# Performance work log

Measured on AMD Instinct MI355X. Metric: run time of the kernel, lower is better.

Reference implementation:

```python
import jax, jax.numpy as jnp
import numpy as np

H = 128      # num_hidden
HIN = 384    # num_in (h_E feature dim)
DFF = 512    # FFN inner dim = 4*H
SCALE = 30.0
EPS = 1e-5

def gelu(x):
    return jax.nn.gelu(x, approximate=False)

def linear(x, w, b):
    return x @ w.T + b

def layer_norm(x, w, b):
    mu = jnp.mean(x, axis=-1, keepdims=True)
    var = jnp.var(x, axis=-1, keepdims=True)
    return (x - mu) * jax.lax.rsqrt(var + EPS) * w + b


def setup_inputs() -> dict:
    key = jax.random.key(0)
    ks = jax.random.split(key, 10)
    B, N, K = 4, 2048, 48
    s = lambda d: 1.0 / np.sqrt(d)
    return {
        "h_V": jax.random.normal(ks[0], (B, N, H), jnp.float32),
        "h_E": jax.random.normal(ks[1], (B, N, K, HIN), jnp.float32),
        "mask_V": jnp.ones((B, N), jnp.float32),
        "mask_attend": jnp.ones((B, N, K), jnp.float32),
        "W1_w": jax.random.normal(ks[2], (H, H + HIN), jnp.float32) * s(H + HIN),
        "W1_b": jnp.zeros((H,), jnp.float32),
        "W2_w": jax.random.normal(ks[3], (H, H), jnp.float32) * s(H),
        "W2_b": jnp.zeros((H,), jnp.float32),
        "W3_w": jax.random.normal(ks[4], (H, H), jnp.float32) * s(H),
        "W3_b": jnp.zeros((H,), jnp.float32),
        "ln1_w": jnp.ones((H,), jnp.float32),
        "ln1_b": jnp.zeros((H,), jnp.float32),
        "Win_w": jax.random.normal(ks[5], (DFF, H), jnp.float32) * s(H),
        "Win_b": jnp.zeros((DFF,), jnp.float32),
        "Wout_w": jax.random.normal(ks[6], (H, DFF), jnp.float32) * s(DFF),
        "Wout_b": jnp.zeros((H,), jnp.float32),
        "ln2_w": jnp.ones((H,), jnp.float32),
        "ln2_b": jnp.zeros((H,), jnp.float32),
    }


def reference(h_V, h_E, mask_V, mask_attend,
              W1_w, W1_b, W2_w, W2_b, W3_w, W3_b,
              ln1_w, ln1_b, Win_w, Win_b, Wout_w, Wout_b, ln2_w, ln2_b):
    K = h_E.shape[-2]
    # broadcast node feats to neighbors and concat: [B, N, K, H+HIN]
    h_V_expand = jnp.broadcast_to(h_V[:, :, None, :], (*h_V.shape[:2], K, h_V.shape[-1]))
    h_EV = jnp.concatenate([h_V_expand, h_E], axis=-1)
    h_message = linear(gelu(linear(gelu(linear(h_EV, W1_w, W1_b)), W2_w, W2_b)), W3_w, W3_b)
    h_message = mask_attend[..., None] * h_message
    dh = jnp.sum(h_message, axis=-2) / SCALE
    h = layer_norm(h_V + dh, ln1_w, ln1_b)
    dh = linear(gelu(linear(h, Win_w, Win_b)), Wout_w, Wout_b)
    h = layer_norm(h + dh, ln2_w, ln2_b)
    return mask_V[..., None] * h
```

## Files before the change

kernel.cpp:

```cpp
#include <hip/hip_runtime.h>
#include <hip/hip_bf16.h>

#define H    128
#define HIN  384
#define FIN  512
#define KNB  48
#define DFF  512
#define NNODES 8192
#define NNB_F (KNB*HIN)

typedef float f32x4 __attribute__((ext_vector_type(4)));
typedef short bf16x8 __attribute__((ext_vector_type(8)));

__device__ __forceinline__ short bfs(float x){
  __hip_bfloat16 h = __float2bfloat16(x);
  return *(short*)&h;
}

__device__ __forceinline__ bf16x8 pack8(float4 a, float4 b){
  bf16x8 o;
  o[0]=bfs(a.x); o[1]=bfs(a.y); o[2]=bfs(a.z); o[3]=bfs(a.w);
  o[4]=bfs(b.x); o[5]=bfs(b.y); o[6]=bfs(b.z); o[7]=bfs(b.w);
  return o;
}

__device__ __forceinline__ float gelu_f(float x){
  float x2 = x*x;
  float z  = x * fmaf(0.0713548162726f, x2, 1.59576912161f);
  z = fminf(fmaxf(z, -30.f), 30.f);
  float e = __expf(z);
  return x * e * __builtin_amdgcn_rcpf(1.f + e);
}

__device__ __forceinline__ f32x4 zero4(){ f32x4 z; z[0]=0.f;z[1]=0.f;z[2]=0.f;z[3]=0.f; return z; }

__global__ __launch_bounds__(256) void k_convert(
    const float* __restrict__ W1, const float* __restrict__ W2,
    const float* __restrict__ W3, const float* __restrict__ Win,
    const float* __restrict__ Wout, unsigned short* __restrict__ dst)
{
  int i0 = (blockIdx.x*256 + threadIdx.x)*4;
  #pragma unroll
  for (int t=0;t<4;t++){
    int idx = i0 + t;
    float v;
    if      (idx <  65536) v = W1[idx];
    else if (idx <  81920) v = W2[idx-65536];
    else if (idx <  98304) v = W3[idx-81920];
    else if (idx < 163840) v = Win[idx-98304];
    else                   v = Wout[idx-163840];
    dst[idx] = (unsigned short)bfs(v);
  }
}

__global__ __launch_bounds__(256) void k_bias1(
    const float* __restrict__ hV, const unsigned short* __restrict__ wW1,
    const float* __restrict__ W1b, float* __restrict__ bias1)
{
  int tid = threadIdx.x;
  int wid = tid>>6, lane = tid&63;
  int lr = lane&15, lg = lane>>4;
  int m0 = (blockIdx.x*4 + wid)*16;

  f32x4 acc[8];
  #pragma unroll
  for (int i=0;i<8;i++) acc[i] = zero4();

  #pragma unroll
  for (int ks=0; ks<4; ks++){
    const float* p = hV + (size_t)(m0+lr)*H + ks*32 + lg*8;
    bf16x8 a = pack8(*(const float4*)p, *(const float4*)(p+4));
    #pragma unroll
    for (int nt=0; nt<8; nt++){
      bf16x8 b = *(const bf16x8*)(wW1 + (size_t)(nt*16+lr)*FIN + ks*32 + lg*8);
      acc[nt] = __builtin_amdgcn_mfma_f32_16x16x32_bf16(a, b, acc[nt], 0,0,0);
    }
  }
  #pragma unroll
  for (int nt=0; nt<8; nt++){
    int col = nt*16 + lr;
    float bv = W1b[col];
    #pragma unroll
    for (int e=0;e<4;e++){
      int row = lg*4 + e;
      bias1[(size_t)(m0+row)*H + col] = acc[nt][e] + bv;
    }
  }
}

__global__ __launch_bounds__(256,5) void k_message(
    const float* __restrict__ hV, const float* __restrict__ hE,
    const float* __restrict__ maskA,
    const unsigned short* __restrict__ wW1, const unsigned short* __restrict__ wW2,
    const unsigned short* __restrict__ wW3,
    const float* __restrict__ W2b, const float* __restrict__ W3b,
    const float* __restrict__ ln1w, const float* __restrict__ ln1b,
    const float* __restrict__ bias1, float* __restrict__ hmid)
{
  __shared__ __align__(16) unsigned short sB0[48*136];
  __shared__ __align__(16) unsigned short sB1[48*136];
  __shared__ float sMask[48];
  __shared__ float sBias[128];
  __shared__ float sDh[128];

  int node = blockIdx.x;
  int tid  = threadIdx.x;
  const float* hEn = hE + (size_t)node * NNB_F;

  int wid = tid>>6, lane = tid&63;
  int lr = lane&15, lg = lane>>4;
  int sr = tid>>4, scg = tid&15;
  const float* gp = hEn + sr*HIN + scg*8;

  float4 pf[3][2];
  #pragma unroll
  for (int i=0;i<3;i++){
    const float* p = gp + i*16*HIN;
    pf[i][0] = *(const float4*)(p); pf[i][1] = *(const float4*)(p+4);
  }
  if (tid < 48)  sMask[tid] = maskA[(size_t)node*KNB + tid];
  if (tid < 128) sBias[tid] = bias1[(size_t)node*H + tid];
  #pragma unroll
  for (int i=0;i<3;i++)
    *(bf16x8*)(&sB0[(sr+16*i)*136 + scg*8]) = pack8(pf[i][0], pf[i][1]);
  __syncthreads();

  f32x4 acc1[3][2];
  #pragma unroll
  for (int mt=0;mt<3;mt++){ acc1[mt][0]=zero4(); acc1[mt][1]=zero4(); }

  auto gemm1_chunk = [&](const unsigned short* buf, int c){
    #pragma unroll
    for (int ks=0; ks<4; ks++){
      bf16x8 a[3];
      #pragma unroll
      for (int mt=0;mt<3;mt++)
        a[mt] = *(const bf16x8*)(buf + (mt*16+lr)*136 + ks*32 + lg*8);
      #pragma unroll
      for (int j=0;j<2;j++){
        int nt = wid*2 + j;
        bf16x8 b = *(const bf16x8*)(wW1 + (size_t)(nt*16+lr)*FIN + (H + c*128 + ks*32 + lg*8));
        #pragma unroll
        for (int mt=0;mt<3;mt++)
          acc1[mt][j] = __builtin_amdgcn_mfma_f32_16x16x32_bf16(a[mt], b, acc1[mt][j], 0,0,0);
      }
    }
  };

  #pragma unroll
  for (int i=0;i<3;i++){
    const float* p = gp + i*16*HIN + 128;
    pf[i][0] = *(const float4*)(p); pf[i][1] = *(const float4*)(p+4);
  }
  gemm1_chunk(sB0, 0);
  #pragma unroll
  for (int i=0;i<3;i++)
    *(bf16x8*)(&sB1[(sr+16*i)*136 + scg*8]) = pack8(pf[i][0], pf[i][1]);
  __syncthreads();

  #pragma unroll
  for (int i=0;i<3;i++){
    const float* p = gp + i*16*HIN + 256;
    pf[i][0] = *(const float4*)(p); pf[i][1] = *(const float4*)(p+4);
  }
  gemm1_chunk(sB1, 1);
  #pragma unroll
  for (int i=0;i<3;i++)
    *(bf16x8*)(&sB0[(sr+16*i)*136 + scg*8]) = pack8(pf[i][0], pf[i][1]);
  __syncthreads();

  gemm1_chunk(sB0, 2);

  #pragma unroll
  for (int j=0;j<2;j++){
    int col = (wid*2+j)*16 + lr;
    float bv = sBias[col];
    #pragma unroll
    for (int mt=0;mt<3;mt++){
      #pragma unroll
      for (int e=0;e<4;e++){
        float g = gelu_f(acc1[mt][j][e] + bv);
        int row = mt*16 + lg*4 + e;
        sB1[row*136 + col] = (unsigned short)bfs(g);
      }
    }
  }
  __syncthreads();

  f32x4 acc2[3][2];
  #pragma unroll
  for (int mt=0;mt<3;mt++){ acc2[mt][0]=zero4(); acc2[mt][1]=zero4(); }
  #pragma unroll
  for (int ks=0; ks<4; ks++){
    bf16x8 a[3];
    #pragma unroll
    for (int mt=0;mt<3;mt++)
      a[mt] = *(const bf16x8*)(sB1 + (mt*16+lr)*136 + ks*32 + lg*8);
    #pragma unroll
    for (int j=0;j<2;j++){
      int nt = wid*2 + j;
      bf16x8 b = *(const bf16x8*)(wW2 + (size_t)(nt*16+lr)*H + ks*32 + lg*8);
      #pragma unroll
      for (int mt=0;mt<3;mt++)
        acc2[mt][j] = __builtin_amdgcn_mfma_f32_16x16x32_bf16(a[mt], b, acc2[mt][j], 0,0,0);
    }
  }
  #pragma unroll
  for (int j=0;j<2;j++){
    int col = (wid*2+j)*16 + lr;
    float bv = W2b[col];
    #pragma unroll
    for (int mt=0;mt<3;mt++){
      #pragma unroll
      for (int e=0;e<4;e++){
        float g = gelu_f(acc2[mt][j][e] + bv);
        int row = mt*16 + lg*4 + e;
        sB0[row*136 + col] = (unsigned short)bfs(g);
      }
    }
  }
  __syncthreads();

  f32x4 acc3[3][2];
  #pragma unroll
  for (int mt=0;mt<3;mt++){ acc3[mt][0]=zero4(); acc3[mt][1]=zero4(); }
  #pragma unroll
  for (int ks=0; ks<4; ks++){
    bf16x8 a[3];
    #pragma unroll
    for (int mt=0;mt<3;mt++)
      a[mt] = *(const bf16x8*)(sB0 + (mt*16+lr)*136 + ks*32 + lg*8);
    #pragma unroll
    for (int j=0;j<2;j++){
      int nt = wid*2 + j;
      bf16x8 b = *(const bf16x8*)(wW3 + (size_t)(nt*16+lr)*H + ks*32 + lg*8);
      #pragma unroll
      for (int mt=0;mt<3;mt++)
        acc3[mt][j] = __builtin_amdgcn_mfma_f32_16x16x32_bf16(a[mt], b, acc3[mt][j], 0,0,0);
    }
  }
  #pragma unroll
  for (int j=0;j<2;j++){
    int col = (wid*2+j)*16 + lr;
    float bv = W3b[col];
    float p = 0.f;
    #pragma unroll
    for (int mt=0;mt<3;mt++){
      #pragma unroll
      for (int e=0;e<4;e++){
        int row = mt*16 + lg*4 + e;
        p += (acc3[mt][j][e] + bv) * sMask[row];
      }
    }
    p += __shfl_xor(p, 16);
    p += __shfl_xor(p, 32);
    if (lane < 16) sDh[(wid*2+j)*16 + lane] = p;
  }
  __syncthreads();

  if (wid == 0){
    int c0i = lane, c1i = lane + 64;
    float t0 = hV[(size_t)node*H + c0i] + sDh[c0i]*(1.0f/30.0f);
    float t1 = hV[(size_t)node*H + c1i] + sDh[c1i]*(1.0f/30.0f);
    float s = t0 + t1, q = t0*t0 + t1*t1;
    #pragma unroll
    for (int off=1; off<64; off<<=1){ s += __shfl_xor(s, off); q += __shfl_xor(q, off); }
    float mu  = s * (1.0f/128.0f);
    float var = q * (1.0f/128.0f) - mu*mu;
    float rs  = rsqrtf(var + 1e-5f);
    hmid[(size_t)node*H + c0i] = (t0-mu)*rs*ln1w[c0i] + ln1b[c0i];
    hmid[(size_t)node*H + c1i] = (t1-mu)*rs*ln1w[c1i] + ln1b[c1i];
  }
}

__global__ __launch_bounds__(256) void k_ffn(
    const float* __restrict__ hmid, const unsigned short* __restrict__ wWin,
    const unsigned short* __restrict__ wWout,
    const float* __restrict__ Winb, const float* __restrict__ Woutb,
    const float* __restrict__ ln2w, const float* __restrict__ ln2b,
    const float* __restrict__ maskV, float* __restrict__ out)
{
  __shared__ __align__(16) unsigned short sH[32*136];
  __shared__ __align__(16) unsigned short sU[32*520];
  __shared__ float sT[32*132];

  int tid = threadIdx.x;
  int m0 = blockIdx.x * 32;

  #pragma unroll
  for (int i=0;i<2;i++){
    int c = i*256 + tid;
    int row = c>>4, cir = c&15;
    const float* p = hmid + (size_t)(m0+row)*H + cir*8;
    *(bf16x8*)(sH + row*136 + cir*8) = pack8(*(const float4*)p, *(const float4*)(p+4));
  }
  __syncthreads();

  int wid = tid>>6, lane = tid&63;
  int lr = lane&15, lg = lane>>4;

  f32x4 acc[2][8];
  #pragma unroll
  for (int mt=0;mt<2;mt++)
    #pragma unroll
    for (int j=0;j<8;j++) acc[mt][j] = zero4();

  #pragma unroll
  for (int ks=0; ks<4; ks++){
    bf16x8 a[2];
    #pragma unroll
    for (int mt=0;mt<2;mt++)
      a[mt] = *(const bf16x8*)(sH + (mt*16+lr)*136 + ks*32 + lg*8);
    #pragma unroll
    for (int j=0;j<8;j++){
      int nt = wid*8 + j;
      bf16x8 b = *(const bf16x8*)(wWin + (size_t)(nt*16+lr)*H + ks*32 + lg*8);
      #pragma unroll
      for (int mt=0;mt<2;mt++)
        acc[mt][j] = __builtin_amdgcn_mfma_f32_16x16x32_bf16(a[mt], b, acc[mt][j], 0,0,0);
    }
  }
  #pragma unroll
  for (int j=0;j<8;j++){
    int col = (wid*8+j)*16 + lr;
    float bv = Winb[col];
    #pragma unroll
    for (int mt=0;mt<2;mt++){
      #pragma unroll
      for (int e=0;e<4;e++){
        float g = gelu_f(acc[mt][j][e] + bv);
        int row = mt*16 + lg*4 + e;
        sU[row*520 + col] = (unsigned short)bfs(g);
      }
    }
  }
  __syncthreads();

  f32x4 accO[2][2];
  #pragma unroll
  for (int mt=0;mt<2;mt++){ accO[mt][0]=zero4(); accO[mt][1]=zero4(); }

  for (int ks=0; ks<16; ks++){
    bf16x8 a[2];
    #pragma unroll
    for (int mt=0;mt<2;mt++)
      a[mt] = *(const bf16x8*)(sU + (mt*16+lr)*520 + ks*32 + lg*8);
    #pragma unroll
    for (int j=0;j<2;j++){
      int nt = wid*2 + j;
      bf16x8 b = *(const bf16x8*)(wWout + (size_t)(nt*16+lr)*DFF + ks*32 + lg*8);
      #pragma unroll
      for (int mt=0;mt<2;mt++)
        accO[mt][j] = __builtin_amdgcn_mfma_f32_16x16x32_bf16(a[mt], b, accO[mt][j], 0,0,0);
    }
  }
  #pragma unroll
  for (int j=0;j<2;j++){
    int col = (wid*2+j)*16 + lr;
    float bv = Woutb[col];
    #pragma unroll
    for (int mt=0;mt<2;mt++){
      #pragma unroll
      for (int e=0;e<4;e++){
        int row = mt*16 + lg*4 + e;
        float t = accO[mt][j][e] + bv + hmid[(size_t)(m0+row)*H + col];
        sT[row*132 + col] = t;
      }
    }
  }
  __syncthreads();

  int row = tid>>3, part = tid&7;
  float s=0.f, q=0.f;
  #pragma unroll
  for (int jj=0;jj<16;jj++){
    float v = sT[row*132 + part*16 + jj];
    s += v; q += v*v;
  }
  s += __shfl_xor(s,1); q += __shfl_xor(q,1);
  s += __shfl_xor(s,2); q += __shfl_xor(q,2);
  s += __shfl_xor(s,4); q += __shfl_xor(q,4);
  float mu  = s*(1.0f/128.0f);
  float var = q*(1.0f/128.0f) - mu*mu;
  float rs  = rsqrtf(var + 1e-5f);
  float mv  = maskV[m0+row];
  #pragma unroll
  for (int jj=0;jj<16;jj++){
    int c = part*16 + jj;
    out[(size_t)(m0+row)*H + c] = mv * ((sT[row*132+c]-mu)*rs*ln2w[c] + ln2b[c]);
  }
}

extern "C" void kernel_launch(void* const* d_in, const int* in_sizes, int n_in,
                              void* d_out, int out_size, void* d_ws, size_t ws_size,
                              hipStream_t stream)
{
  const float* hV    = (const float*)d_in[0];
  const float* hE    = (const float*)d_in[1];
  const float* maskV = (const float*)d_in[2];
  const float* maskA = (const float*)d_in[3];
  const float* W1w   = (const float*)d_in[4];
  const float* W1b   = (const float*)d_in[5];
  const float* W2w   = (const float*)d_in[6];
  const float* W2b   = (const float*)d_in[7];
  const float* W3w   = (const float*)d_in[8];
  const float* W3b   = (const float*)d_in[9];
  const float* ln1w  = (const float*)d_in[10];
  const float* ln1b  = (const float*)d_in[11];
  const float* Winw  = (const float*)d_in[12];
  const float* Winb  = (const float*)d_in[13];
  const float* Woutw = (const float*)d_in[14];
  const float* Woutb = (const float*)d_in[15];
  const float* ln2w  = (const float*)d_in[16];
  const float* ln2b  = (const float*)d_in[17];

  unsigned short* wAll  = (unsigned short*)d_ws;
  unsigned short* wW1   = wAll;
  unsigned short* wW2   = wAll + 65536;
  unsigned short* wW3   = wAll + 81920;
  unsigned short* wWin  = wAll + 98304;
  unsigned short* wWout = wAll + 163840;
  float* bias1 = (float*)((char*)d_ws + 458752);
  float* hmid  = (float*)d_out;
  float* outp  = (float*)d_out;

  k_convert<<<224, 256, 0, stream>>>(W1w, W2w, W3w, Winw, Woutw, wAll);
  k_bias1  <<<128, 256, 0, stream>>>(hV, wW1, W1b, bias1);
  k_message<<<NNODES, 256, 0, stream>>>(hV, hE, maskA, wW1, wW2, wW3,
                                        W2b, W3b, ln1w, ln1b, bias1, hmid);
  k_ffn    <<<NNODES/32, 256, 0, stream>>>(hmid, wWin, wWout, Winb, Woutb,
                                           ln2w, ln2b, maskV, outp);
}
```

Before: 249.7 us.

## Assign one node per wavefront in message kernel, replacing block barriers with wave fences

Each wavefront now processes a whole node on its own: all 128 output columns per GEMM, with a private LDS tile. This replaces the block-wide __syncthreads and the shared double buffer with wave-local LDS fences, and the grid shrinks by four. The goal is to remove block-level synchronisation stalls and let each wave stream its own h_E. The cost is 96 accumulator registers per wave (launch bounds lowered to 3), and the global loads are no longer prefetched ahead of the MFMA work.

```diff
diff --git a/kernel.cpp b/kernel.cpp
--- a/kernel.cpp
+++ b/kernel.cpp
@@ -33,6 +33,11 @@
 }
 
 __device__ __forceinline__ f32x4 zero4(){ f32x4 z; z[0]=0.f;z[1]=0.f;z[2]=0.f;z[3]=0.f; return z; }
+
+__device__ __forceinline__ void wave_lds_fence(){
+  asm volatile("s_waitcnt lgkmcnt(0)" ::: "memory");
+  __builtin_amdgcn_wave_barrier();
+}
 
 __global__ __launch_bounds__(256) void k_convert(
     const float* __restrict__ W1, const float* __restrict__ W2,
@@ -88,7 +93,7 @@
   }
 }
 
-__global__ __launch_bounds__(256,5) void k_message(
+__global__ __launch_bounds__(256,3) void k_message(
     const float* __restrict__ hV, const float* __restrict__ hE,
     const float* __restrict__ maskA,
     const unsigned short* __restrict__ wW1, const unsigned short* __restrict__ wW2,
@@ -97,168 +102,148 @@
     const float* __restrict__ ln1w, const float* __restrict__ ln1b,
     const float* __restrict__ bias1, float* __restrict__ hmid)
 {
-  __shared__ __align__(16) unsigned short sB0[48*136];
-  __shared__ __align__(16) unsigned short sB1[48*136];
-  __shared__ float sMask[48];
-  __shared__ float sBias[128];
-  __shared__ float sDh[128];
-
-  int node = blockIdx.x;
+  __shared__ __align__(16) unsigned short sWave[4][48*136];
+
   int tid  = threadIdx.x;
+  int wid  = tid>>6, lane = tid&63;
+  int node = blockIdx.x*4 + wid;
+  unsigned short* sG = sWave[wid];
+
+  int lr = lane&15, lg = lane>>4;
+  int srow = lane>>4, scol = lane&15;
   const float* hEn = hE + (size_t)node * NNB_F;
 
-  int wid = tid>>6, lane = tid&63;
-  int lr = lane&15, lg = lane>>4;
-  int sr = tid>>4, scg = tid&15;
-  const float* gp = hEn + sr*HIN + scg*8;
-
-  float4 pf[3][2];
-  #pragma unroll
-  for (int i=0;i<3;i++){
-    const float* p = gp + i*16*HIN;
-    pf[i][0] = *(const float4*)(p); pf[i][1] = *(const float4*)(p+4);
-  }
-  if (tid < 48)  sMask[tid] = maskA[(size_t)node*KNB + tid];
-  if (tid < 128) sBias[tid] = bias1[(size_t)node*H + tid];
-  #pragma unroll
-  for (int i=0;i<3;i++)
-    *(bf16x8*)(&sB0[(sr+16*i)*136 + scg*8]) = pack8(pf[i][0], pf[i][1]);
-  __syncthreads();
-
-  f32x4 acc1[3][2];
-  #pragma unroll
-  for (int mt=0;mt<3;mt++){ acc1[mt][0]=zero4(); acc1[mt][1]=zero4(); }
-
-  auto gemm1_chunk = [&](const unsigned short* buf, int c){
+  f32x4 acc[3][8];
+  #pragma unroll
+  for (int mt=0;mt<3;mt++)
+    #pragma unroll
+    for (int nt=0;nt<8;nt++) acc[mt][nt] = zero4();
+
+  for (int c=0;c<3;++c){
+    const float* cp = hEn + c*128 + scol*8;
+    #pragma unroll
+    for (int i=0;i<12;i++){
+      int row = srow + 4*i;
+      const float* p = cp + (size_t)row*HIN;
+      float4 a0 = *(const float4*)p, a1 = *(const float4*)(p+4);
+      *(bf16x8*)(sG + row*136 + scol*8) = pack8(a0, a1);
+    }
+    wave_lds_fence();
+
     #pragma unroll
     for (int ks=0; ks<4; ks++){
       bf16x8 a[3];
       #pragma unroll
       for (int mt=0;mt<3;mt++)
-        a[mt] = *(const bf16x8*)(buf + (mt*16+lr)*136 + ks*32 + lg*8);
-      #pragma unroll
-      for (int j=0;j<2;j++){
-        int nt = wid*2 + j;
+        a[mt] = *(const bf16x8*)(sG + (mt*16+lr)*136 + ks*32 + lg*8);
+      #pragma unroll
+      for (int nt=0;nt<8;nt++){
         bf16x8 b = *(const bf16x8*)(wW1 + (size_t)(nt*16+lr)*FIN + (H + c*128 + ks*32 + lg*8));
         #pragma unroll
         for (int mt=0;mt<3;mt++)
-          acc1[mt][j] = __builtin_amdgcn_mfma_f32_16x16x32_bf16(a[mt], b, acc1[mt][j], 0,0,0);
+          acc[mt][nt] = __builtin_amdgcn_mfma_f32_16x16x32_bf16(a[mt], b, acc[mt][nt], 0,0,0);
       }
     }
-  };
-
-  #pragma unroll
-  for (int i=0;i<3;i++){
-    const float* p = gp + i*16*HIN + 128;
-    pf[i][0] = *(const float4*)(p); pf[i][1] = *(const float4*)(p+4);
-  }
-  gemm1_chunk(sB0, 0);
-  #pragma unroll
-  for (int i=0;i<3;i++)
-    *(bf16x8*)(&sB1[(sr+16*i)*136 + scg*8]) = pack8(pf[i][0], pf[i][1]);
-  __syncthreads();
-
-  #pragma unroll
-  for (int i=0;i<3;i++){
-    const float* p = gp + i*16*HIN + 256;
-    pf[i][0] = *(const float4*)(p); pf[i][1] = *(const float4*)(p+4);
-  }
-  gemm1_chunk(sB1, 1);
-  #pragma unroll
-  for (int i=0;i<3;i++)
-    *(bf16x8*)(&sB0[(sr+16*i)*136 + scg*8]) = pack8(pf[i][0], pf[i][1]);
-  __syncthreads();
-
-  gemm1_chunk(sB0, 2);
-
-  #pragma unroll
-  for (int j=0;j<2;j++){
-    int col = (wid*2+j)*16 + lr;
-    float bv = sBias[col];
-    #pragma unroll
-    for (int mt=0;mt<3;mt++){
+    wave_lds_fence();
+  }
+
+  #pragma unroll
+  for (int nt=0;nt<8;nt++){
+    float bv = bias1[(size_t)node*H + nt*16 + lr];
+    #pragma unroll
+    for (int mt=0;mt<3;mt++)
       #pragma unroll
       for (int e=0;e<4;e++){
-        float g = gelu_f(acc1[mt][j][e] + bv);
-        int row = mt*16 + lg*4 + e;
-        sB1[row*136 + col] = (unsigned short)bfs(g);
+        float g = gelu_f(acc[mt][nt][e] + bv);
+        sG[(mt*16+lg*4+e)*136 + nt*16+lr] = (unsigned short)bfs(g);
       }
-    }
-  }
-  __syncthreads();
-
-  f32x4 acc2[3][2];
-  #pragma unroll
-  for (int mt=0;mt<3;mt++){ acc2[mt][0]=zero4(); acc2[mt][1]=zero4(); }
+  }
+  wave_lds_fence();
+
+  f32x4 acc2[3][8];
+  #pragma unroll
+  for (int mt=0;mt<3;mt++)
+    #pragma unroll
+    for (int nt=0;nt<8;nt++) acc2[mt][nt] = zero4();
   #pragma unroll
   for (int ks=0; ks<4; ks++){
     bf16x8 a[3];
     #pragma unroll
     for (int mt=0;mt<3;mt++)
-      a[mt] = *(const bf16x8*)(sB1 + (mt*16+lr)*136 + ks*32 + lg*8);
-    #pragma unroll
-    for (int j=0;j<2;j++){
-      int nt = wid*2 + j;
+      a[mt] = *(const bf16x8*)(sG + (mt*16+lr)*136 + ks*32 + lg*8);
+    #pragma unroll
+    for (int nt=0;nt<8;nt++){
       bf16x8 b = *(const bf16x8*)(wW2 + (size_t)(nt*16+lr)*H + ks*32 + lg*8);
       #pragma unroll
       for (int mt=0;mt<3;mt++)
-        acc2[mt][j] = __builtin_amdgcn_mfma_f32_16x16x32_bf16(a[mt], b, acc2[mt][j], 0,0,0);
-    }
-  }
-  #pragma unroll
-  for (int j=0;j<2;j++){
-    int col = (wid*2+j)*16 + lr;
-    float bv = W2b[col];
-    #pragma unroll
-    for (int mt=0;mt<3;mt++){
+        acc2[mt][nt] = __builtin_amdgcn_mfma_f32_16x16x32_bf16(a[mt], b, acc2[mt][nt], 0,0,0);
+    }
+  }
+  wave_lds_fence();
+
+  #pragma unroll
+  for (int nt=0;nt<8;nt++){
+    float bv = W2b[nt*16 + lr];
+    #pragma unroll
+    for (int mt=0;mt<3;mt++)
       #pragma unroll
       for (int e=0;e<4;e++){
-        float g = gelu_f(acc2[mt][j][e] + bv);
-        int row = mt*16 + lg*4 + e;
-        sB0[row*136 + col] = (unsigned short)bfs(g);
+        float g = gelu_f(acc2[mt][nt][e] + bv);
+        sG[(mt*16+lg*4+e)*136 + nt*16+lr] = (unsigned short)bfs(g);
       }
-    }
-  }
-  __syncthreads();
-
-  f32x4 acc3[3][2];
-  #pragma unroll
-  for (int mt=0;mt<3;mt++){ acc3[mt][0]=zero4(); acc3[mt][1]=zero4(); }
+  }
+  wave_lds_fence();
+
+  f32x4 acc3[3][8];
+  #pragma unroll
+  for (int mt=0;mt<3;mt++)
+    #pragma unroll
+    for (int nt=0;nt<8;nt++) acc3[mt][nt] = zero4();
   #pragma unroll
   for (int ks=0; ks<4; ks++){
     bf16x8 a[3];
     #pragma unroll
     for (int mt=0;mt<3;mt++)
-      a[mt] = *(const bf16x8*)(sB0 + (mt*16+lr)*136 + ks*32 + lg*8);
-    #pragma unroll
-    for (int j=0;j<2;j++){
-      int nt = wid*2 + j;
+      a[mt] = *(const bf16x8*)(sG + (mt*16+lr)*136 + ks*32 + lg*8);
+    #pragma unroll
+    for (int nt=0;nt<8;nt++){
       bf16x8 b = *(const bf16x8*)(wW3 + (size_t)(nt*16+lr)*H + ks*32 + lg*8);
       #pragma unroll
       for (int mt=0;mt<3;mt++)
-        acc3[mt][j] = __builtin_amdgcn_mfma_f32_16x16x32_bf16(a[mt], b, acc3[mt][j], 0,0,0);
-    }
-  }
-  #pragma unroll
-  for (int j=0;j<2;j++){
-    int col = (wid*2+j)*16 + lr;
-    float bv = W3b[col];
+        acc3[mt][nt] = __builtin_amdgcn_mfma_f32_16x16x32_bf16(a[mt], b, acc3[mt][nt], 0,0,0);
+    }
+  }
+  wave_lds_fence();
+
+  float mv[3][4];
+  #pragma unroll
+  for (int mt=0;mt<3;mt++)
+    #pragma unroll
+    for (int e=0;e<4;e++)
+      mv[mt][e] = maskA[(size_t)node*KNB + mt*16 + lg*4 + e];
+
+  float pn[8];
+  #pragma unroll
+  for (int nt=0;nt<8;nt++){
+    float bv = W3b[nt*16 + lr];
     float p = 0.f;
     #pragma unroll
-    for (int mt=0;mt<3;mt++){
-      #pragma unroll
-      for (int e=0;e<4;e++){
-        int row = mt*16 + lg*4 + e;
-        p += (acc3[mt][j][e] + bv) * sMask[row];
-      }
-    }
+    for (int mt=0;mt<3;mt++)
+      #pragma unroll
+      for (int e=0;e<4;e++)
+        p += (acc3[mt][nt][e] + bv) * mv[mt][e];
     p += __shfl_xor(p, 16);
     p += __shfl_xor(p, 32);
-    if (lane < 16) sDh[(wid*2+j)*16 + lane] = p;
-  }
-  __syncthreads();
-
-  if (wid == 0){
+    pn[nt] = p;
+  }
+  float* sDh = (float*)sG;
+  if (lane < 16){
+    #pragma unroll
+    for (int nt=0;nt<8;nt++) sDh[nt*16 + lane] = pn[nt];
+  }
+  wave_lds_fence();
+
+  {
     int c0i = lane, c1i = lane + 64;
     float t0 = hV[(size_t)node*H + c0i] + sDh[c0i]*(1.0f/30.0f);
     float t1 = hV[(size_t)node*H + c1i] + sDh[c1i]*(1.0f/30.0f);
@@ -426,8 +411,8 @@
 
   k_convert<<<224, 256, 0, stream>>>(W1w, W2w, W3w, Winw, Woutw, wAll);
   k_bias1  <<<128, 256, 0, stream>>>(hV, wW1, W1b, bias1);
-  k_message<<<NNODES, 256, 0, stream>>>(hV, hE, maskA, wW1, wW2, wW3,
-                                        W2b, W3b, ln1w, ln1b, bias1, hmid);
+  k_message<<<NNODES/4, 256, 0, stream>>>(hV, hE, maskA, wW1, wW2, wW3,
+                                          W2b, W3b, ln1w, ln1b, bias1, hmid);
   k_ffn    <<<NNODES/32, 256, 0, stream>>>(hmid, wWin, wWout, Winb, Woutb,
                                            ln2w, ln2b, maskV, outp);
 }
```

After: 318.5 us. +27.6%, slower.

## Process four nodes per message block with cross-node prefetch of edge features

Applied to the files above, without the earlier changes.

The message kernel becomes persistent over NB=4 nodes per block, looping with two ping-pong shared buffers. It prefetches the first h_E chunk of the next node into registers during the current node's later GEMM stages, hiding load latency across the node boundary. Mask and bias1 are now read directly from global memory instead of being staged in shared memory. The grid shrinks fourfold, which lowers launch and prologue cost but reduces parallelism and may raise register pressure under the 5-wave launch bound.

```diff
diff --git a/kernel.cpp b/kernel.cpp
--- a/kernel.cpp
+++ b/kernel.cpp
@@ -8,6 +8,7 @@
 #define DFF  512
 #define NNODES 8192
 #define NNB_F (KNB*HIN)
+#define NB   4
 
 typedef float f32x4 __attribute__((ext_vector_type(4)));
 typedef short bf16x8 __attribute__((ext_vector_type(8)));
@@ -97,179 +98,198 @@
     const float* __restrict__ ln1w, const float* __restrict__ ln1b,
     const float* __restrict__ bias1, float* __restrict__ hmid)
 {
-  __shared__ __align__(16) unsigned short sB0[48*136];
-  __shared__ __align__(16) unsigned short sB1[48*136];
-  __shared__ float sMask[48];
-  __shared__ float sBias[128];
+  __shared__ __align__(16) unsigned short sX[48*136];
+  __shared__ __align__(16) unsigned short sY[48*136];
   __shared__ float sDh[128];
 
-  int node = blockIdx.x;
   int tid  = threadIdx.x;
-  const float* hEn = hE + (size_t)node * NNB_F;
-
-  int wid = tid>>6, lane = tid&63;
+  int wid  = tid>>6, lane = tid&63;
   int lr = lane&15, lg = lane>>4;
   int sr = tid>>4, scg = tid&15;
-  const float* gp = hEn + sr*HIN + scg*8;
-
+
+  int node0 = blockIdx.x*NB;
+  const float* gp0 = hE + (size_t)node0*NNB_F + sr*HIN + scg*8;
+
+  unsigned short* bS = sX;
+  unsigned short* bT = sY;
   float4 pf[3][2];
+
   #pragma unroll
   for (int i=0;i<3;i++){
-    const float* p = gp + i*16*HIN;
-    pf[i][0] = *(const float4*)(p); pf[i][1] = *(const float4*)(p+4);
-  }
-  if (tid < 48)  sMask[tid] = maskA[(size_t)node*KNB + tid];
-  if (tid < 128) sBias[tid] = bias1[(size_t)node*H + tid];
+    const float* p = gp0 + i*16*HIN;
+    pf[i][0]=*(const float4*)p; pf[i][1]=*(const float4*)(p+4);
+  }
   #pragma unroll
   for (int i=0;i<3;i++)
-    *(bf16x8*)(&sB0[(sr+16*i)*136 + scg*8]) = pack8(pf[i][0], pf[i][1]);
+    *(bf16x8*)(bS + (sr+16*i)*136 + scg*8) = pack8(pf[i][0], pf[i][1]);
   __syncthreads();
 
-  f32x4 acc1[3][2];
-  #pragma unroll
-  for (int mt=0;mt<3;mt++){ acc1[mt][0]=zero4(); acc1[mt][1]=zero4(); }
-
-  auto gemm1_chunk = [&](const unsigned short* buf, int c){
+  for (int it=0; it<NB; ++it){
+    int node = node0 + it;
+    const float* gp = gp0 + (size_t)it*NNB_F;
+
+    f32x4 acc1[3][2];
+    #pragma unroll
+    for (int mt=0;mt<3;mt++){ acc1[mt][0]=zero4(); acc1[mt][1]=zero4(); }
+
+    auto gemm1_chunk = [&](const unsigned short* buf, int c){
+      #pragma unroll
+      for (int ks=0; ks<4; ks++){
+        bf16x8 a[3];
+        #pragma unroll
+        for (int mt=0;mt<3;mt++)
+          a[mt] = *(const bf16x8*)(buf + (mt*16+lr)*136 + ks*32 + lg*8);
+        #pragma unroll
+        for (int j=0;j<2;j++){
+          int nt = wid*2 + j;
+          bf16x8 b = *(const bf16x8*)(wW1 + (size_t)(nt*16+lr)*FIN + (H + c*128 + ks*32 + lg*8));
+          #pragma unroll
+          for (int mt=0;mt<3;mt++)
+            acc1[mt][j] = __builtin_amdgcn_mfma_f32_16x16x32_bf16(a[mt], b, acc1[mt][j], 0,0,0);
+        }
+      }
+    };
+
+    #pragma unroll
+    for (int i=0;i<3;i++){
+      const float* p = gp + i*16*HIN + 128;
+      pf[i][0]=*(const float4*)p; pf[i][1]=*(const float4*)(p+4);
+    }
+    gemm1_chunk(bS, 0);
+    #pragma unroll
+    for (int i=0;i<3;i++)
+      *(bf16x8*)(bT + (sr+16*i)*136 + scg*8) = pack8(pf[i][0], pf[i][1]);
+    __syncthreads();
+
+    #pragma unroll
+    for (int i=0;i<3;i++){
+      const float* p = gp + i*16*HIN + 256;
+      pf[i][0]=*(const float4*)p; pf[i][1]=*(const float4*)(p+4);
+    }
+    gemm1_chunk(bT, 1);
+    #pragma unroll
+    for (int i=0;i<3;i++)
+      *(bf16x8*)(bS + (sr+16*i)*136 + scg*8) = pack8(pf[i][0], pf[i][1]);
+    __syncthreads();
+
+    gemm1_chunk(bS, 2);
+    if (it < NB-1){
+      const float* gn = gp + NNB_F;
+      #pragma unroll
+      for (int i=0;i<3;i++){
+        const float* p = gn + i*16*HIN;
+        pf[i][0]=*(const float4*)p; pf[i][1]=*(const float4*)(p+4);
+      }
+    }
+
+    #pragma unroll
+    for (int j=0;j<2;j++){
+      int col = (wid*2+j)*16 + lr;
+      float bv = bias1[(size_t)node*H + col];
+      #pragma unroll
+      for (int mt=0;mt<3;mt++)
+        #pragma unroll
+        for (int e=0;e<4;e++){
+          float g = gelu_f(acc1[mt][j][e] + bv);
+          bT[(mt*16+lg*4+e)*136 + col] = (unsigned short)bfs(g);
+        }
+    }
+    __syncthreads();
+
+    f32x4 acc2[3][2];
+    #pragma unroll
+    for (int mt=0;mt<3;mt++){ acc2[mt][0]=zero4(); acc2[mt][1]=zero4(); }
     #pragma unroll
     for (int ks=0; ks<4; ks++){
       bf16x8 a[3];
       #pragma unroll
       for (int mt=0;mt<3;mt++)
-        a[mt] = *(const bf16x8*)(buf + (mt*16+lr)*136 + ks*32 + lg*8);
+        a[mt] = *(const bf16x8*)(bT + (mt*16+lr)*136 + ks*32 + lg*8);
       #pragma unroll
       for (int j=0;j<2;j++){
         int nt = wid*2 + j;
-        bf16x8 b = *(const bf16x8*)(wW1 + (size_t)(nt*16+lr)*FIN + (H + c*128 + ks*32 + lg*8));
+        bf16x8 b = *(const bf16x8*)(wW2 + (size_t)(nt*16+lr)*H + ks*32 + lg*8);
         #pragma unroll
         for (int mt=0;mt<3;mt++)
-          acc1[mt][j] = __builtin_amdgcn_mfma_f32_16x16x32_bf16(a[mt], b, acc1[mt][j], 0,0,0);
-      }
-    }
-  };
-
-  #pragma unroll
-  for (int i=0;i<3;i++){
-    const float* p = gp + i*16*HIN + 128;
-    pf[i][0] = *(const float4*)(p); pf[i][1] = *(const float4*)(p+4);
-  }
-  gemm1_chunk(sB0, 0);
-  #pragma unroll
-  for (int i=0;i<3;i++)
-    *(bf16x8*)(&sB1[(sr+16*i)*136 + scg*8]) = pack8(pf[i][0], pf[i][1]);
-  __syncthreads();
-
-  #pragma unroll
-  for (int i=0;i<3;i++){
-    const float* p = gp + i*16*HIN + 256;
-    pf[i][0] = *(const float4*)(p); pf[i][1] = *(const float4*)(p+4);
-  }
-  gemm1_chunk(sB1, 1);
-  #pragma unroll
-  for (int i=0;i<3;i++)
-    *(bf16x8*)(&sB0[(sr+16*i)*136 + scg*8]) = pack8(pf[i][0], pf[i][1]);
-  __syncthreads();
-
-  gemm1_chunk(sB0, 2);
-
-  #pragma unroll
-  for (int j=0;j<2;j++){
-    int col = (wid*2+j)*16 + lr;
-    float bv = sBias[col];
-    #pragma unroll
-    for (int mt=0;mt<3;mt++){
-      #pragma unroll
-      for (int e=0;e<4;e++){
-        float g = gelu_f(acc1[mt][j][e] + bv);
-        int row = mt*16 + lg*4 + e;
-        sB1[row*136 + col] = (unsigned short)bfs(g);
-      }
-    }
-  }
-  __syncthreads();
-
-  f32x4 acc2[3][2];
-  #pragma unroll
-  for (int mt=0;mt<3;mt++){ acc2[mt][0]=zero4(); acc2[mt][1]=zero4(); }
-  #pragma unroll
-  for (int ks=0; ks<4; ks++){
-    bf16x8 a[3];
+          acc2[mt][j] = __builtin_amdgcn_mfma_f32_16x16x32_bf16(a[mt], b, acc2[mt][j], 0,0,0);
+      }
+    }
+
+    #pragma unroll
+    for (int j=0;j<2;j++){
+      int col = (wid*2+j)*16 + lr;
+      float bv = W2b[col];
+      #pragma unroll
+      for (int mt=0;mt<3;mt++)
+        #pragma unroll
+        for (int e=0;e<4;e++){
+          float g = gelu_f(acc2[mt][j][e] + bv);
+          bS[(mt*16+lg*4+e)*136 + col] = (unsigned short)bfs(g);
+        }
+    }
+    __syncthreads();
+
+    f32x4 acc3[3][2];
+    #pragma unroll
+    for (int mt=0;mt<3;mt++){ acc3[mt][0]=zero4(); acc3[mt][1]=zero4(); }
+    #pragma unroll
+    for (int ks=0; ks<4; ks++){
+      bf16x8 a[3];
+      #pragma unroll
+      for (int mt=0;mt<3;mt++)
+        a[mt] = *(const bf16x8*)(bS + (mt*16+lr)*136 + ks*32 + lg*8);
+      #pragma unroll
+      for (int j=0;j<2;j++){
+        int nt = wid*2 + j;
+        bf16x8 b = *(const bf16x8*)(wW3 + (size_t)(nt*16+lr)*H + ks*32 + lg*8);
+        #pragma unroll
+        for (int mt=0;mt<3;mt++)
+          acc3[mt][j] = __builtin_amdgcn_mfma_f32_16x16x32_bf16(a[mt], b, acc3[mt][j], 0,0,0);
+      }
+    }
+    if (it < NB-1){
+      #pragma unroll
+      for (int i=0;i<3;i++)
+        *(bf16x8*)(bT + (sr+16*i)*136 + scg*8) = pack8(pf[i][0], pf[i][1]);
+    }
+
+    float mvv[3][4];
     #pragma unroll
     for (int mt=0;mt<3;mt++)
-      a[mt] = *(const bf16x8*)(sB1 + (mt*16+lr)*136 + ks*32 + lg*8);
+      #pragma unroll
+      for (int e=0;e<4;e++)
+        mvv[mt][e] = maskA[(size_t)node*KNB + mt*16 + lg*4 + e];
     #pragma unroll
     for (int j=0;j<2;j++){
-      int nt = wid*2 + j;
-      bf16x8 b = *(const bf16x8*)(wW2 + (size_t)(nt*16+lr)*H + ks*32 + lg*8);
+      int col = (wid*2+j)*16 + lr;
+      float bv = W3b[col];
+      float p = 0.f;
       #pragma unroll
       for (int mt=0;mt<3;mt++)
-        acc2[mt][j] = __builtin_amdgcn_mfma_f32_16x16x32_bf16(a[mt], b, acc2[mt][j], 0,0,0);
-    }
-  }
-  #pragma unroll
-  for (int j=0;j<2;j++){
-    int col = (wid*2+j)*16 + lr;
-    float bv = W2b[col];
-    #pragma unroll
-    for (int mt=0;mt<3;mt++){
-      #pragma unroll
-      for (int e=0;e<4;e++){
-        float g = gelu_f(acc2[mt][j][e] + bv);
-        int row = mt*16 + lg*4 + e;
-        sB0[row*136 + col] = (unsigned short)bfs(g);
-      }
-    }
-  }
-  __syncthreads();
-
-  f32x4 acc3[3][2];
-  #pragma unroll
-  for (int mt=0;mt<3;mt++){ acc3[mt][0]=zero4(); acc3[mt][1]=zero4(); }
-  #pragma unroll
-  for (int ks=0; ks<4; ks++){
-    bf16x8 a[3];
-    #pragma unroll
-    for (int mt=0;mt<3;mt++)
-      a[mt] = *(const bf16x8*)(sB0 + (mt*16+lr)*136 + ks*32 + lg*8);
-    #pragma unroll
-    for (int j=0;j<2;j++){
-      int nt = wid*2 + j;
-      bf16x8 b = *(const bf16x8*)(wW3 + (size_t)(nt*16+lr)*H + ks*32 + lg*8);
-      #pragma unroll
-      for (int mt=0;mt<3;mt++)
-        acc3[mt][j] = __builtin_amdgcn_mfma_f32_16x16x32_bf16(a[mt], b, acc3[mt][j], 0,0,0);
-    }
-  }
-  #pragma unroll
-  for (int j=0;j<2;j++){
-    int col = (wid*2+j)*16 + lr;
-    float bv = W3b[col];
-    float p = 0.f;
-    #pragma unroll
-    for (int mt=0;mt<3;mt++){
-      #pragma unroll
-      for (int e=0;e<4;e++){
-        int row = mt*16 + lg*4 + e;
-        p += (acc3[mt][j][e] + bv) * sMask[row];
-      }
-    }
-    p += __shfl_xor(p, 16);
-    p += __shfl_xor(p, 32);
-    if (lane < 16) sDh[(wid*2+j)*16 + lane] = p;
-  }
-  __syncthreads();
-
-  if (wid == 0){
-    int c0i = lane, c1i = lane + 64;
-    float t0 = hV[(size_t)node*H + c0i] + sDh[c0i]*(1.0f/30.0f);
-    float t1 = hV[(size_t)node*H + c1i] + sDh[c1i]*(1.0f/30.0f);
-    float s = t0 + t1, q = t0*t0 + t1*t1;
-    #pragma unroll
-    for (int off=1; off<64; off<<=1){ s += __shfl_xor(s, off); q += __shfl_xor(q, off); }
-    float mu  = s * (1.0f/128.0f);
-    float var = q * (1.0f/128.0f) - mu*mu;
-    float rs  = rsqrtf(var + 1e-5f);
-    hmid[(size_t)node*H + c0i] = (t0-mu)*rs*ln1w[c0i] + ln1b[c0i];
-    hmid[(size_t)node*H + c1i] = (t1-mu)*rs*ln1w[c1i] + ln1b[c1i];
+        #pragma unroll
+        for (int e=0;e<4;e++)
+          p += (acc3[mt][j][e] + bv) * mvv[mt][e];
+      p += __shfl_xor(p, 16);
+      p += __shfl_xor(p, 32);
+      if (lane < 16) sDh[(wid*2+j)*16 + lane] = p;
+    }
+    __syncthreads();
+
+    if (wid == 0){
+      int c0i = lane, c1i = lane + 64;
+      float t0 = hV[(size_t)node*H + c0i] + sDh[c0i]*(1.0f/30.0f);
+      float t1 = hV[(size_t)node*H + c1i] + sDh[c1i]*(1.0f/30.0f);
+      float s = t0 + t1, q = t0*t0 + t1*t1;
+      #pragma unroll
+      for (int off=1; off<64; off<<=1){ s += __shfl_xor(s, off); q += __shfl_xor(q, off); }
+      float mu  = s * (1.0f/128.0f);
+      float var = q * (1.0f/128.0f) - mu*mu;
+      float rs  = rsqrtf(var + 1e-5f);
+      hmid[(size_t)node*H + c0i] = (t0-mu)*rs*ln1w[c0i] + ln1b[c0i];
+      hmid[(size_t)node*H + c1i] = (t1-mu)*rs*ln1w[c1i] + ln1b[c1i];
+    }
+
+    unsigned short* tmp = bS; bS = bT; bT = tmp;
   }
 }
 
@@ -426,8 +446,8 @@
 
   k_convert<<<224, 256, 0, stream>>>(W1w, W2w, W3w, Winw, Woutw, wAll);
   k_bias1  <<<128, 256, 0, stream>>>(hV, wW1, W1b, bias1);
-  k_message<<<NNODES, 256, 0, stream>>>(hV, hE, maskA, wW1, wW2, wW3,
-                                        W2b, W3b, ln1w, ln1b, bias1, hmid);
+  k_message<<<NNODES/NB, 256, 0, stream>>>(hV, hE, maskA, wW1, wW2, wW3,
+                                           W2b, W3b, ln1w, ln1b, bias1, hmid);
   k_ffn    <<<NNODES/32, 256, 0, stream>>>(hmid, wWin, wWout, Winb, Woutb,
                                            ln2w, ln2b, maskV, outp);
 }
```

Measured after the change: 488.5 us. 1.96x slower.
